# Kernel tuning notes

Hardware: AMD Instinct MI355X
Metric: run time of the kernel (lower is better)

The kernel has to match this reference:

```python
import jax, jax.numpy as jnp
import numpy as np

EPS = 1e-6
H = 12  # num_attention_heads

def _phi(x):
    # feature map used by fast-transformers LinearAttention: elu(x) + 1
    return jax.nn.elu(x) + 1.0

def setup_inputs() -> dict:
    key = jax.random.key(0)
    k1, k2, k3 = jax.random.split(key, 3)
    B, N, D = 32, 1024, 768
    x = jax.random.normal(k1, (B, N, D), dtype=jnp.float32)
    W_qkv = jax.random.normal(k2, (D, 3 * D), dtype=jnp.float32) * (D ** -0.5)
    W_out = jax.random.normal(k3, (D, D), dtype=jnp.float32) * (D ** -0.5)
    b_out = jnp.zeros((D,), dtype=jnp.float32)
    return {"x": x, "W_qkv": W_qkv, "W_out": W_out, "b_out": b_out}

def reference(x, W_qkv, W_out, b_out):
    B, N, D = x.shape
    d = D // H
    # F.pad(x, [0,0,0,1]): append one zero token along sequence
    x_ = jnp.pad(x, ((0, 0), (0, 1), (0, 0)))              # [B, N+1, D]
    qkv = x_ @ W_qkv                                        # [B, N+1, 3D]
    q, k, v = jnp.split(qkv, 3, axis=-1)
    q = q.reshape(B, N + 1, H, d)
    k = k.reshape(B, N + 1, H, d)
    v = v.reshape(B, N + 1, H, d)
    # non-causal linear attention (mask is all-ones -> no masking)
    q = _phi(q)
    k = _phi(k)
    kv = jnp.einsum('bshd,bshm->bhdm', k, v)                # [B, H, d, d]
    z = 1.0 / (jnp.einsum('blhd,bhd->blh', q, k.sum(axis=1)) + EPS)
    out = jnp.einsum('blhd,bhdm,blh->blhm', q, kv, z)       # [B, N+1, H, d]
    out = out.reshape(B, N + 1, D)
    out = out @ W_out + b_out                               # dropout = identity (eval)
    return out[:, :-1, :]                                   # drop padding token
```

## Files before the change

kernel.cpp:

```cpp
#include <hip/hip_runtime.h>
#include <hip/hip_bf16.h>


typedef __bf16 bf16x8 __attribute__((ext_vector_type(8)));
typedef float f32x4 __attribute__((ext_vector_type(4)));

__device__ __forceinline__ ushort f2bf(float f) {
  union { float f; unsigned u; } x; x.f = f;
  unsigned r = x.u + 0x7fffu + ((x.u >> 16) & 1u);
  return (ushort)(r >> 16);
}
__device__ __forceinline__ float bf2f(ushort h) {
  union { unsigned u; float f; } x; x.u = ((unsigned)h) << 16;
  return x.f;
}
__device__ __forceinline__ float bits2f(unsigned u) {
  union { unsigned u; float f; } x; x.u = u;
  return x.f;
}
__device__ __forceinline__ void gload_lds16(const void* g, void* lds) {
  __builtin_amdgcn_global_load_lds((const __attribute__((address_space(1))) void*)g,
                                   (__attribute__((address_space(3))) void*)lds, 16, 0, 0);
}
__device__ __forceinline__ bf16x8 ds_read128(const ushort* p) {
  bf16x8 r;
  asm volatile("ds_read_b128 %0, %1"
               : "=v"(r)
               : "v"((const __attribute__((address_space(3))) ushort*)p));
  return r;
}

__global__ __launch_bounds__(256) void cvt_f32_bf16(const float* __restrict__ in,
                                                    ushort* __restrict__ out, int n4) {
  int i = blockIdx.x * 256 + threadIdx.x;
  if (i >= n4) return;
  float4 v = reinterpret_cast<const float4*>(in)[i];
  ushort4 o;
  o.x = f2bf(v.x); o.y = f2bf(v.y); o.z = f2bf(v.z); o.w = f2bf(v.w);
  reinterpret_cast<ushort4*>(out)[i] = o;
}

__global__ __launch_bounds__(256) void transpose_cvt(const float* __restrict__ src,
                                                     ushort* __restrict__ dst, int R, int C) {
  __shared__ float tile[32][33];
  int bc = blockIdx.x * 32, br = blockIdx.y * 32;
  int tx = threadIdx.x & 31, ty = threadIdx.x >> 5;
  #pragma unroll
  for (int i = 0; i < 32; i += 8)
    tile[ty + i][tx] = src[(size_t)(br + ty + i) * C + (bc + tx)];
  __syncthreads();
  #pragma unroll
  for (int i = 0; i < 32; i += 8)
    dst[(size_t)(bc + ty + i) * R + (br + tx)] = f2bf(tile[tx][ty + i]);
}

template <int MODE>
__global__ __launch_bounds__(512, 2) void gemm256(const ushort* __restrict__ A,
                                                  const ushort* __restrict__ Bt,
                                                  void* __restrict__ C,
                                                  const float* __restrict__ bias,
                                                  int N, int K, int nbx, int cpx) {
  extern __shared__ ushort lds[];
  const int tid = threadIdx.x;
  const int lane = tid & 63;
  const int wid = tid >> 6;
  const int wm = wid >> 2, wn = wid & 3;
  const int laneR = lane & 15, laneS = lane >> 4;

  const int bid = blockIdx.x;
  const int lin = (bid & 7) * cpx + (bid >> 3);
  const int by = lin / nbx, bx = lin - by * nbx;
  const int m0 = by * 256, n0 = bx * 256;
  const int NT = K >> 6;

  const int sr = tid >> 2, ss = tid & 3;
  const int sslot = ss ^ ((sr >> 1) & 3);
  const ushort* Asrc0 = A + (size_t)(m0 + sr) * K + sslot * 8;
  const ushort* Bsrc0 = Bt + (size_t)(n0 + sr) * K + sslot * 8;
  const size_t rowstep = (size_t)128 * K;
  const int ldst0 = tid * 8;

  const int sprime = laneS ^ ((laneR >> 1) & 3);
  const int aoff = (wm * 128 + laneR) * 32 + sprime * 8;
  const int boff = 16384 + (wn * 64 + laneR) * 32 + sprime * 8;

  f32x4 acc[8][4] = {};
  bf16x8 afrX[4], afrY[4], bfrX[4], bfrY[4];

  #define STAGE_HT(SRC, KT, KS, DST)                                              \
    { gload_lds16((SRC) + (KT) * 64 + (KS) * 32,                                  \
                  (DST) + (KS) * 8192 + ldst0);                                   \
      gload_lds16((SRC) + (KT) * 64 + (KS) * 32 + rowstep,                        \
                  (DST) + (KS) * 8192 + 4096 + ldst0); }
  #define SBAR  __builtin_amdgcn_sched_barrier(0)
  #define MFMA16(ACCBASE, AF, BF)                                                 \
    _Pragma("unroll")                                                             \
    for (int ii = 0; ii < 4; ++ii)                                                \
      _Pragma("unroll")                                                           \
      for (int j = 0; j < 4; ++j)                                                 \
        acc[(ACCBASE) + ii][j] =                                                  \
            __builtin_amdgcn_mfma_f32_16x16x32_bf16(AF[ii], BF[j], acc[(ACCBASE) + ii][j], 0, 0, 0);

  {
    ushort* b0 = lds;
    ushort* b1 = lds + 32768;
    STAGE_HT(Asrc0, 0, 0, b0);
    STAGE_HT(Bsrc0, 0, 0, b0 + 16384);
    STAGE_HT(Asrc0, 0, 1, b0);
    STAGE_HT(Bsrc0, 0, 1, b0 + 16384);
    STAGE_HT(Asrc0, 1, 0, b1);
    STAGE_HT(Bsrc0, 1, 0, b1 + 16384);
  }
  asm volatile("s_waitcnt vmcnt(8)" ::: "memory");
  SBAR;
  __builtin_amdgcn_s_barrier();
  SBAR;
  #pragma unroll
  for (int j = 0; j < 4; ++j)
    bfrX[j] = *(const bf16x8*)(lds + boff + j * 512);
  #pragma unroll
  for (int ii = 0; ii < 4; ++ii)
    afrX[ii] = *(const bf16x8*)(lds + aoff + ii * 512);

  for (int t = 0; t < NT; ++t) {
    ushort* cbuf = lds + (t & 1) * 32768;
    ushort* nbuf = lds + ((t & 1) ^ 1) * 32768;
    const int t1 = (t + 1 < NT) ? t + 1 : t;
    const int t2 = (t + 2 < NT) ? t + 2 : t;

    STAGE_HT(Asrc0, t1, 1, nbuf);
    asm volatile("s_waitcnt vmcnt(6)" ::: "memory");
    SBAR;
    #pragma unroll
    for (int ii = 0; ii < 4; ++ii)
      afrY[ii] = *(const bf16x8*)(cbuf + aoff + (4 + ii) * 512);
    SBAR;
    __builtin_amdgcn_s_setprio(1);
    MFMA16(0, afrX, bfrX);
    __builtin_amdgcn_s_setprio(0);
    SBAR;
    __builtin_amdgcn_s_barrier();
    SBAR;

    STAGE_HT(Bsrc0, t1, 1, nbuf + 16384);
    SBAR;
    #pragma unroll
    for (int j = 0; j < 4; ++j)
      bfrY[j] = *(const bf16x8*)(cbuf + 8192 + boff + j * 512);
    #pragma unroll
    for (int ii = 0; ii < 4; ++ii)
      afrX[ii] = *(const bf16x8*)(cbuf + 8192 + aoff + ii * 512);
    SBAR;
    __builtin_amdgcn_s_setprio(1);
    MFMA16(4, afrY, bfrX);
    __builtin_amdgcn_s_setprio(0);
    SBAR;
    __builtin_amdgcn_s_barrier();
    SBAR;

    STAGE_HT(Asrc0, t2, 0, cbuf);
    asm volatile("s_waitcnt vmcnt(6)" ::: "memory");
    SBAR;
    #pragma unroll
    for (int ii = 0; ii < 4; ++ii)
      afrY[ii] = *(const bf16x8*)(cbuf + 8192 + aoff + (4 + ii) * 512);
    SBAR;
    __builtin_amdgcn_s_setprio(1);
    MFMA16(0, afrX, bfrY);
    __builtin_amdgcn_s_setprio(0);
    SBAR;
    __builtin_amdgcn_s_barrier();
    SBAR;

    STAGE_HT(Bsrc0, t2, 0, cbuf + 16384);
    SBAR;
    #pragma unroll
    for (int j = 0; j < 4; ++j)
      bfrX[j] = *(const bf16x8*)(nbuf + boff + j * 512);
    #pragma unroll
    for (int ii = 0; ii < 4; ++ii)
      afrX[ii] = *(const bf16x8*)(nbuf + aoff + ii * 512);
    SBAR;
    __builtin_amdgcn_s_setprio(1);
    MFMA16(4, afrY, bfrY);
    __builtin_amdgcn_s_setprio(0);
    SBAR;
    __builtin_amdgcn_s_barrier();
    SBAR;
  }
  #undef STAGE_HT
  #undef MFMA16
  asm volatile("s_waitcnt vmcnt(0)" ::: "memory");

  #pragma unroll
  for (int i = 0; i < 8; ++i) {
    const int grow0 = m0 + wm * 128 + i * 16 + (laneS << 2);
    #pragma unroll
    for (int j = 0; j < 4; ++j) {
      const int gcol = n0 + wn * 64 + j * 16 + laneR;
      #pragma unroll
      for (int r = 0; r < 4; ++r) {
        float v = acc[i][j][r];
        if (MODE == 0) {
          if (gcol < 1536) v = (v > 0.f) ? (v + 1.f) : __expf(v);
          reinterpret_cast<ushort*>(C)[(size_t)(grow0 + r) * N + gcol] = f2bf(v);
        } else {
          reinterpret_cast<float*>(C)[(size_t)(grow0 + r) * N + gcol] = v + bias[gcol];
        }
      }
    }
  }
}

template <int MODE, int MFR>
__global__ __launch_bounds__(512, 2) void gemm2ph(const ushort* __restrict__ A,
                                                  const ushort* __restrict__ Bt,
                                                  void* __restrict__ C,
                                                  const float* __restrict__ bias,
                                                  int N, int K, int nbx, int cpx) {
  constexpr int BM   = MFR * 32;
  constexpr int ALD  = MFR / 4;
  constexpr int AKS  = BM * 32;
  constexpr int BBASE = BM * 64;
  constexpr int BUFS = (BM + 256) * 64;
  extern __shared__ ushort lds[];
  const int tid = threadIdx.x;
  const int lane = tid & 63;
  const int wid = tid >> 6;
  const int wm = wid >> 2, wn = wid & 3;
  const int laneR = lane & 15, laneS = lane >> 4;

  const int bid = blockIdx.x;
  const int lin = (bid & 7) * cpx + (bid >> 3);
  const int by = lin / nbx, bx = lin - by * nbx;
  const int m0 = by * BM, n0 = bx * 256;
  const int NT = K >> 6;

  const int sr = tid >> 2, ss = tid & 3;
  const int sslot = ss ^ ((sr >> 1) & 3);
  const ushort* Asrc0 = A + (size_t)(m0 + sr) * K + sslot * 8;
  const ushort* Bsrc0 = Bt + (size_t)(n0 + sr) * K + sslot * 8;
  const size_t rowstep = (size_t)128 * K;
  const int ldst0 = tid * 8;

  const int sprime = laneS ^ ((laneR >> 1) & 3);
  const int aoff = (wm * (MFR * 16) + laneR) * 32 + sprime * 8;
  const int boff = BBASE + (wn * 64 + laneR) * 32 + sprime * 8;

  f32x4 acc[MFR][4] = {};
  bf16x8 afr[MFR], bfr[4];

  #define STAGE_K(KT, KS, DB)                                                     \
    { _Pragma("unroll")                                                           \
      for (int L = 0; L < ALD; ++L)                                               \
        gload_lds16(Asrc0 + (KT) * 64 + (KS) * 32 + (size_t)L * rowstep,          \
                    lds + (DB) + (KS) * AKS + L * 4096 + ldst0);                  \
      _Pragma("unroll")                                                           \
      for (int L = 0; L < 2; ++L)                                                 \
        gload_lds16(Bsrc0 + (KT) * 64 + (KS) * 32 + (size_t)L * rowstep,          \
                    lds + (DB) + BBASE + (KS) * 8192 + L * 4096 + ldst0); }
  #define SBAR  __builtin_amdgcn_sched_barrier(0)
  #define VMCNT_WAIT                                                              \
    if constexpr (MFR == 8) asm volatile("s_waitcnt vmcnt(8)" ::: "memory");      \
    else                    asm volatile("s_waitcnt vmcnt(6)" ::: "memory");
  #define PHASE_SYNC                                                              \
    SBAR;                                                                         \
    __builtin_amdgcn_s_barrier();                                                 \
    asm volatile("s_waitcnt lgkmcnt(0)");                                         \
    SBAR;
  #define PHASE_END                                                               \
    SBAR;                                                                         \
    __builtin_amdgcn_s_barrier();                                                 \
    SBAR;
  #define MFMA_CL                                                                 \
    __builtin_amdgcn_s_setprio(1);                                                \
    _Pragma("unroll")                                                             \
    for (int ii = 0; ii < MFR; ++ii)                                              \
      _Pragma("unroll")                                                           \
      for (int j = 0; j < 4; ++j)                                                 \
        acc[ii][j] =                                                              \
            __builtin_amdgcn_mfma_f32_16x16x32_bf16(afr[ii], bfr[j], acc[ii][j], 0, 0, 0); \
    __builtin_amdgcn_s_setprio(0);

  STAGE_K(0, 0, 0);
  STAGE_K(0, 1, 0);
  STAGE_K(1, 0, BUFS);
  VMCNT_WAIT;
  SBAR;
  __builtin_amdgcn_s_barrier();
  SBAR;

  for (int t = 0; t < NT; ++t) {
    const int cb = (t & 1) * BUFS;
    const int nb = BUFS - cb;
    const int t1 = (t + 1 < NT) ? t + 1 : t;
    const int t2 = (t + 2 < NT) ? t + 2 : t;

    #pragma unroll
    for (int j = 0; j < 4; ++j) bfr[j] = ds_read128(lds + cb + boff + j * 512);
    #pragma unroll
    for (int ii = 0; ii < MFR; ++ii) afr[ii] = ds_read128(lds + cb + aoff + ii * 512);
    STAGE_K(t1, 1, nb);
    VMCNT_WAIT;
    PHASE_SYNC;
    MFMA_CL;
    PHASE_END;

    #pragma unroll
    for (int j = 0; j < 4; ++j) bfr[j] = ds_read128(lds + cb + 8192 + boff + j * 512);
    #pragma unroll
    for (int ii = 0; ii < MFR; ++ii) afr[ii] = ds_read128(lds + cb + AKS + aoff + ii * 512);
    STAGE_K(t2, 0, cb);
    VMCNT_WAIT;
    PHASE_SYNC;
    MFMA_CL;
    PHASE_END;
  }
  #undef STAGE_K
  #undef MFMA_CL
  #undef PHASE_SYNC
  #undef PHASE_END
  #undef VMCNT_WAIT
  asm volatile("s_waitcnt vmcnt(0)" ::: "memory");

  #pragma unroll
  for (int i = 0; i < MFR; ++i) {
    const int grow0 = m0 + wm * (MFR * 16) + i * 16 + (laneS << 2);
    #pragma unroll
    for (int j = 0; j < 4; ++j) {
      const int gcol = n0 + wn * 64 + j * 16 + laneR;
      #pragma unroll
      for (int r = 0; r < 4; ++r) {
        float v = acc[i][j][r];
        if (MODE == 0) {
          if (gcol < 1536) v = (v > 0.f) ? (v + 1.f) : __expf(v);
          reinterpret_cast<ushort*>(C)[(size_t)(grow0 + r) * N + gcol] = f2bf(v);
        } else {
          reinterpret_cast<float*>(C)[(size_t)(grow0 + r) * N + gcol] = v + bias[gcol];
        }
      }
    }
  }
}

__global__ __launch_bounds__(256) void kv_partial(const ushort* __restrict__ qkv,
                                                  float* __restrict__ kv_part,
                                                  float* __restrict__ ks_part) {
  const int blk = blockIdx.x;
  const int bh = blk >> 2, sp = blk & 3;
  const int b = bh / 12, h = bh % 12;
  const int tid = threadIdx.x;
  __shared__ float Ks[32 * 68];
  __shared__ float Vs[32 * 68];
  float acc[4][4] = {};
  float kacc[4] = {};
  const int dq0 = (tid & 15) * 4, mq0 = (tid >> 4) * 4;
  const int r = tid >> 3, o = (tid & 7) * 8;
  for (int st = 0; st < 256; st += 32) {
    const size_t rowbase = (size_t)(b * 1024 + sp * 256 + st + r) * 2304 + h * 64 + o;
    int4 kraw = *reinterpret_cast<const int4*>(qkv + rowbase + 768);
    int4 vraw = *reinterpret_cast<const int4*>(qkv + rowbase + 1536);
    float kf[8], vf[8];
    {
      const unsigned* kw = reinterpret_cast<const unsigned*>(&kraw);
      const unsigned* vw = reinterpret_cast<const unsigned*>(&vraw);
      #pragma unroll
      for (int w = 0; w < 4; ++w) {
        kf[2 * w]     = bits2f(kw[w] << 16);
        kf[2 * w + 1] = bits2f(kw[w] & 0xffff0000u);
        vf[2 * w]     = bits2f(vw[w] << 16);
        vf[2 * w + 1] = bits2f(vw[w] & 0xffff0000u);
      }
    }
    __syncthreads();
    #pragma unroll
    for (int w = 0; w < 8; ++w) {
      Ks[r * 68 + o + w] = kf[w];
      Vs[r * 68 + o + w] = vf[w];
    }
    __syncthreads();
    #pragma unroll 8
    for (int s = 0; s < 32; ++s) {
      f32x4 kk = *reinterpret_cast<const f32x4*>(&Ks[s * 68 + dq0]);
      f32x4 vv = *reinterpret_cast<const f32x4*>(&Vs[s * 68 + mq0]);
      #pragma unroll
      for (int jm = 0; jm < 4; ++jm)
        #pragma unroll
        for (int id = 0; id < 4; ++id)
          acc[jm][id] += vv[jm] * kk[id];
      if (mq0 == 0) {
        #pragma unroll
        for (int id = 0; id < 4; ++id) kacc[id] += kk[id];
      }
    }
  }
  float* kvp = kv_part + ((size_t)sp * 384 + bh) * 4096;
  #pragma unroll
  for (int jm = 0; jm < 4; ++jm)
    #pragma unroll
    for (int id = 0; id < 4; ++id)
      kvp[(mq0 + jm) * 64 + dq0 + id] = acc[jm][id];
  if (mq0 == 0) {
    #pragma unroll
    for (int id = 0; id < 4; ++id)
      ks_part[((size_t)sp * 384 + bh) * 64 + dq0 + id] = kacc[id];
  }
}

__global__ __launch_bounds__(256) void kv_reduce(const float* __restrict__ kv_part,
                                                 const float* __restrict__ ks_part,
                                                 ushort* __restrict__ kv_bf,
                                                 float* __restrict__ ksum) {
  int i = blockIdx.x * 256 + threadIdx.x;
  if (i < 384 * 4096) {
    float s = 0.f;
    #pragma unroll
    for (int p = 0; p < 4; ++p) s += kv_part[(size_t)p * (384 * 4096) + i];
    kv_bf[i] = f2bf(s);
  }
  if (i < 384 * 64) {
    float s = 1.0f;
    #pragma unroll
    for (int p = 0; p < 4; ++p) s += ks_part[(size_t)p * (384 * 64) + i];
    ksum[i] = s;
  }
}

__global__ __launch_bounds__(256) void attn_kernel(const ushort* __restrict__ qkv,
                                                   const ushort* __restrict__ kv_bf,
                                                   const float* __restrict__ ksum,
                                                   ushort* __restrict__ attn) {
  const int blk = blockIdx.x;
  const int bh = blk >> 3, tb = blk & 7;
  const int b = bh / 12, h = bh % 12;
  const int row0 = b * 1024 + tb * 128;
  __shared__ ushort Qs[128 * 64];
  __shared__ ushort KVs[64 * 64];
  __shared__ float zs[128];
  __shared__ float ks_lds[64];
  const int tid = threadIdx.x;
  const int lane = tid & 63, w = tid >> 6;
  #pragma unroll
  for (int j = 0; j < 4; ++j) {
    int c = j * 256 + tid;
    gload_lds16(qkv + (size_t)(row0 + (c >> 3)) * 2304 + h * 64 + (c & 7) * 8, &Qs[c * 8]);
  }
  #pragma unroll
  for (int j = 0; j < 2; ++j) {
    int c = j * 256 + tid;
    gload_lds16(kv_bf + (size_t)bh * 4096 + c * 8, &KVs[c * 8]);
  }
  if (tid < 64) ks_lds[tid] = ksum[bh * 64 + tid];
  asm volatile("s_waitcnt vmcnt(0)" ::: "memory");
  __syncthreads();
  if (tid < 128) {
    float d = 0.f;
    #pragma unroll 8
    for (int e = 0; e < 64; ++e) d += bf2f(Qs[tid * 64 + e]) * ks_lds[e];
    zs[tid] = 1.f / (d + 1e-6f);
  }
  __syncthreads();
  f32x4 acc[2][4] = {};
  #pragma unroll
  for (int ks = 0; ks < 2; ++ks) {
    bf16x8 a[2], bb[4];
    #pragma unroll
    for (int i = 0; i < 2; ++i)
      a[i] = *reinterpret_cast<const bf16x8*>(&Qs[(w * 32 + i * 16 + (lane & 15)) * 64 + ks * 32 + (lane >> 4) * 8]);
    #pragma unroll
    for (int j = 0; j < 4; ++j)
      bb[j] = *reinterpret_cast<const bf16x8*>(&KVs[(j * 16 + (lane & 15)) * 64 + ks * 32 + (lane >> 4) * 8]);
    #pragma unroll
    for (int i = 0; i < 2; ++i)
      #pragma unroll
      for (int j = 0; j < 4; ++j)
        acc[i][j] = __builtin_amdgcn_mfma_f32_16x16x32_bf16(a[i], bb[j], acc[i][j], 0, 0, 0);
  }
  #pragma unroll
  for (int i = 0; i < 2; ++i) {
    const int t0 = w * 32 + i * 16 + ((lane >> 4) << 2);
    #pragma unroll
    for (int j = 0; j < 4; ++j) {
      const int m = j * 16 + (lane & 15);
      #pragma unroll
      for (int r = 0; r < 4; ++r) {
        float v = acc[i][j][r] * zs[t0 + r];
        attn[(size_t)(row0 + t0 + r) * 768 + h * 64 + m] = f2bf(v);
      }
    }
  }
}

extern "C" void kernel_launch(void* const* d_in, const int* in_sizes, int n_in,
                              void* d_out, int out_size, void* d_ws, size_t ws_size,
                              hipStream_t stream) {
  (void)in_sizes; (void)n_in; (void)out_size; (void)ws_size;
  const float* x    = (const float*)d_in[0];
  const float* Wqkv = (const float*)d_in[1];
  const float* Wout = (const float*)d_in[2];
  const float* bout = (const float*)d_in[3];
  float* out = (float*)d_out;
  char* ws = (char*)d_ws;

  ushort* xbf    = (ushort*)(ws);
  ushort* wqkvT  = (ushort*)(ws + 50331648);
  ushort* woutT  = (ushort*)(ws + 53870592);
  ushort* qkv    = (ushort*)(ws + 55050240);
  float*  ksp    = (float*) (ws + 206045184);
  ushort* kvbf   = (ushort*)(ws + 206438400);
  float*  ksum   = (float*) (ws + 209584128);
  float*  kvpart = (float*)(ws);
  ushort* attn   = (ushort*)(ws);

  static const int LDS1 = 131072;
  static const int LDS2 = 98304;
  hipFuncSetAttribute(reinterpret_cast<const void*>(&gemm256<0>),
                      hipFuncAttributeMaxDynamicSharedMemorySize, LDS1);
  hipFuncSetAttribute(reinterpret_cast<const void*>(&gemm2ph<1, 4>),
                      hipFuncAttributeMaxDynamicSharedMemorySize, LDS2);

  cvt_f32_bf16<<<24576, 256, 0, stream>>>(x, xbf, 6291456);
  transpose_cvt<<<dim3(72, 24), 256, 0, stream>>>(Wqkv, wqkvT, 768, 2304);
  transpose_cvt<<<dim3(24, 24), 256, 0, stream>>>(Wout, woutT, 768, 768);
  gemm256<0><<<1152, 512, LDS1, stream>>>(xbf, wqkvT, qkv, nullptr, 2304, 768, 9, 144);
  kv_partial<<<1536, 256, 0, stream>>>(qkv, kvpart, ksp);
  kv_reduce<<<6144, 256, 0, stream>>>(kvpart, ksp, kvbf, ksum);
  attn_kernel<<<3072, 256, 0, stream>>>(qkv, kvbf, ksum, attn);
  gemm2ph<1, 4><<<768, 512, LDS2, stream>>>(attn, woutT, out, bout, 768, 768, 3, 96);
}
```

Before: 304.1 us.

## Replace 256x256 QKV GEMM with 64x256 tiles loading B directly into registers

The QKV projection GEMM moves from 256x256 tiles with 8 waves and both operands staged in LDS to 64x256 tiles with 4 waves. In the new kernel only A goes through LDS, and each wave loads its B fragments straight from global memory into registers. The aim is more blocks, higher occupancy and less LDS pressure and barrier cost. In exchange, global and L2 traffic for B rises because it is reused across fewer rows, and arithmetic intensity per block drops.

```diff
diff --git a/kernel.cpp b/kernel.cpp
--- a/kernel.cpp
+++ b/kernel.cpp
@@ -27,6 +27,13 @@
   asm volatile("ds_read_b128 %0, %1"
                : "=v"(r)
                : "v"((const __attribute__((address_space(3))) ushort*)p));
+  return r;
+}
+__device__ __forceinline__ bf16x8 gload128(const ushort* p) {
+  bf16x8 r;
+  asm volatile("global_load_dwordx4 %0, %1, off"
+               : "=v"(r)
+               : "v"(p));
   return r;
 }
 
@@ -55,146 +62,105 @@
 }
 
 template <int MODE>
-__global__ __launch_bounds__(512, 2) void gemm256(const ushort* __restrict__ A,
-                                                  const ushort* __restrict__ Bt,
-                                                  void* __restrict__ C,
-                                                  const float* __restrict__ bias,
-                                                  int N, int K, int nbx, int cpx) {
-  extern __shared__ ushort lds[];
+__global__ __launch_bounds__(256, 3) void gemm64(const ushort* __restrict__ A,
+                                                 const ushort* __restrict__ Bt,
+                                                 void* __restrict__ C,
+                                                 const float* __restrict__ bias,
+                                                 int N, int K, int nbx, int cpx) {
+  __shared__ ushort As[2][4096];
   const int tid = threadIdx.x;
   const int lane = tid & 63;
-  const int wid = tid >> 6;
-  const int wm = wid >> 2, wn = wid & 3;
+  const int wn = tid >> 6;
   const int laneR = lane & 15, laneS = lane >> 4;
 
   const int bid = blockIdx.x;
   const int lin = (bid & 7) * cpx + (bid >> 3);
   const int by = lin / nbx, bx = lin - by * nbx;
-  const int m0 = by * 256, n0 = bx * 256;
+  const int m0 = by * 64, n0 = bx * 256;
   const int NT = K >> 6;
 
   const int sr = tid >> 2, ss = tid & 3;
   const int sslot = ss ^ ((sr >> 1) & 3);
-  const ushort* Asrc0 = A + (size_t)(m0 + sr) * K + sslot * 8;
-  const ushort* Bsrc0 = Bt + (size_t)(n0 + sr) * K + sslot * 8;
-  const size_t rowstep = (size_t)128 * K;
-  const int ldst0 = tid * 8;
+  const ushort* Asrc = A + (size_t)(m0 + sr) * K + sslot * 8;
+  const int ldst = tid * 8;
 
   const int sprime = laneS ^ ((laneR >> 1) & 3);
-  const int aoff = (wm * 128 + laneR) * 32 + sprime * 8;
-  const int boff = 16384 + (wn * 64 + laneR) * 32 + sprime * 8;
-
-  f32x4 acc[8][4] = {};
-  bf16x8 afrX[4], afrY[4], bfrX[4], bfrY[4];
-
-  #define STAGE_HT(SRC, KT, KS, DST)                                              \
-    { gload_lds16((SRC) + (KT) * 64 + (KS) * 32,                                  \
-                  (DST) + (KS) * 8192 + ldst0);                                   \
-      gload_lds16((SRC) + (KT) * 64 + (KS) * 32 + rowstep,                        \
-                  (DST) + (KS) * 8192 + 4096 + ldst0); }
+  const int aoff = laneR * 32 + sprime * 8;
+
+  const ushort* Bb0 = Bt + (size_t)(n0 + wn * 64 + laneR) * K + laneS * 8;
+  const size_t jstep = (size_t)16 * K;
+
+  f32x4 acc[4][4] = {};
+  bf16x8 afr[4], bfrX[4], bfrY[4];
+
   #define SBAR  __builtin_amdgcn_sched_barrier(0)
-  #define MFMA16(ACCBASE, AF, BF)                                                 \
+  #define MFMA16(AF, BF)                                                          \
+    __builtin_amdgcn_s_setprio(1);                                                \
     _Pragma("unroll")                                                             \
     for (int ii = 0; ii < 4; ++ii)                                                \
       _Pragma("unroll")                                                           \
       for (int j = 0; j < 4; ++j)                                                 \
-        acc[(ACCBASE) + ii][j] =                                                  \
-            __builtin_amdgcn_mfma_f32_16x16x32_bf16(AF[ii], BF[j], acc[(ACCBASE) + ii][j], 0, 0, 0);
-
-  {
-    ushort* b0 = lds;
-    ushort* b1 = lds + 32768;
-    STAGE_HT(Asrc0, 0, 0, b0);
-    STAGE_HT(Bsrc0, 0, 0, b0 + 16384);
-    STAGE_HT(Asrc0, 0, 1, b0);
-    STAGE_HT(Bsrc0, 0, 1, b0 + 16384);
-    STAGE_HT(Asrc0, 1, 0, b1);
-    STAGE_HT(Bsrc0, 1, 0, b1 + 16384);
-  }
-  asm volatile("s_waitcnt vmcnt(8)" ::: "memory");
+        acc[ii][j] =                                                              \
+            __builtin_amdgcn_mfma_f32_16x16x32_bf16(AF[ii], BF[j], acc[ii][j], 0, 0, 0); \
+    __builtin_amdgcn_s_setprio(0);
+
+  gload_lds16(Asrc,      &As[0][0]    + ldst);
+  gload_lds16(Asrc + 32, &As[0][2048] + ldst);
+  gload_lds16(Asrc + 64, &As[1][0]    + ldst);
+  #pragma unroll
+  for (int j = 0; j < 4; ++j)
+    bfrX[j] = gload128(Bb0 + (size_t)j * jstep);
+  asm volatile("s_waitcnt vmcnt(0)" ::: "memory");
   SBAR;
   __builtin_amdgcn_s_barrier();
   SBAR;
-  #pragma unroll
-  for (int j = 0; j < 4; ++j)
-    bfrX[j] = *(const bf16x8*)(lds + boff + j * 512);
-  #pragma unroll
-  for (int ii = 0; ii < 4; ++ii)
-    afrX[ii] = *(const bf16x8*)(lds + aoff + ii * 512);
 
   for (int t = 0; t < NT; ++t) {
-    ushort* cbuf = lds + (t & 1) * 32768;
-    ushort* nbuf = lds + ((t & 1) ^ 1) * 32768;
+    ushort* cb = &As[t & 1][0];
+    ushort* nb = &As[(t & 1) ^ 1][0];
     const int t1 = (t + 1 < NT) ? t + 1 : t;
     const int t2 = (t + 2 < NT) ? t + 2 : t;
 
-    STAGE_HT(Asrc0, t1, 1, nbuf);
+    #pragma unroll
+    for (int i = 0; i < 4; ++i)
+      afr[i] = ds_read128(cb + aoff + i * 512);
+    #pragma unroll
+    for (int j = 0; j < 4; ++j)
+      bfrY[j] = gload128(Bb0 + (size_t)j * jstep + t * 64 + 32);
+    gload_lds16(Asrc + t1 * 64 + 32, nb + 2048 + ldst);
     asm volatile("s_waitcnt vmcnt(6)" ::: "memory");
     SBAR;
-    #pragma unroll
-    for (int ii = 0; ii < 4; ++ii)
-      afrY[ii] = *(const bf16x8*)(cbuf + aoff + (4 + ii) * 512);
-    SBAR;
-    __builtin_amdgcn_s_setprio(1);
-    MFMA16(0, afrX, bfrX);
-    __builtin_amdgcn_s_setprio(0);
-    SBAR;
     __builtin_amdgcn_s_barrier();
-    SBAR;
-
-    STAGE_HT(Bsrc0, t1, 1, nbuf + 16384);
-    SBAR;
+    asm volatile("s_waitcnt lgkmcnt(0)");
+    SBAR;
+    MFMA16(afr, bfrX);
+    SBAR;
+    __builtin_amdgcn_s_barrier();
+    SBAR;
+
+    #pragma unroll
+    for (int i = 0; i < 4; ++i)
+      afr[i] = ds_read128(cb + 2048 + aoff + i * 512);
     #pragma unroll
     for (int j = 0; j < 4; ++j)
-      bfrY[j] = *(const bf16x8*)(cbuf + 8192 + boff + j * 512);
-    #pragma unroll
-    for (int ii = 0; ii < 4; ++ii)
-      afrX[ii] = *(const bf16x8*)(cbuf + 8192 + aoff + ii * 512);
-    SBAR;
-    __builtin_amdgcn_s_setprio(1);
-    MFMA16(4, afrY, bfrX);
-    __builtin_amdgcn_s_setprio(0);
+      bfrX[j] = gload128(Bb0 + (size_t)j * jstep + t1 * 64);
+    gload_lds16(Asrc + t2 * 64, cb + ldst);
+    asm volatile("s_waitcnt vmcnt(6)" ::: "memory");
     SBAR;
     __builtin_amdgcn_s_barrier();
-    SBAR;
-
-    STAGE_HT(Asrc0, t2, 0, cbuf);
-    asm volatile("s_waitcnt vmcnt(6)" ::: "memory");
-    SBAR;
-    #pragma unroll
-    for (int ii = 0; ii < 4; ++ii)
-      afrY[ii] = *(const bf16x8*)(cbuf + 8192 + aoff + (4 + ii) * 512);
-    SBAR;
-    __builtin_amdgcn_s_setprio(1);
-    MFMA16(0, afrX, bfrY);
-    __builtin_amdgcn_s_setprio(0);
+    asm volatile("s_waitcnt lgkmcnt(0)");
+    SBAR;
+    MFMA16(afr, bfrY);
     SBAR;
     __builtin_amdgcn_s_barrier();
     SBAR;
-
-    STAGE_HT(Bsrc0, t2, 0, cbuf + 16384);
-    SBAR;
-    #pragma unroll
-    for (int j = 0; j < 4; ++j)
-      bfrX[j] = *(const bf16x8*)(nbuf + boff + j * 512);
-    #pragma unroll
-    for (int ii = 0; ii < 4; ++ii)
-      afrX[ii] = *(const bf16x8*)(nbuf + aoff + ii * 512);
-    SBAR;
-    __builtin_amdgcn_s_setprio(1);
-    MFMA16(4, afrY, bfrY);
-    __builtin_amdgcn_s_setprio(0);
-    SBAR;
-    __builtin_amdgcn_s_barrier();
-    SBAR;
-  }
-  #undef STAGE_HT
+  }
   #undef MFMA16
   asm volatile("s_waitcnt vmcnt(0)" ::: "memory");
 
   #pragma unroll
-  for (int i = 0; i < 8; ++i) {
-    const int grow0 = m0 + wm * 128 + i * 16 + (laneS << 2);
+  for (int i = 0; i < 4; ++i) {
+    const int grow0 = m0 + i * 16 + (laneS << 2);
     #pragma unroll
     for (int j = 0; j < 4; ++j) {
       const int gcol = n0 + wn * 64 + j * 16 + laneR;
@@ -259,7 +225,6 @@
       for (int L = 0; L < 2; ++L)                                                 \
         gload_lds16(Bsrc0 + (KT) * 64 + (KS) * 32 + (size_t)L * rowstep,          \
                     lds + (DB) + BBASE + (KS) * 8192 + L * 4096 + ldst0); }
-  #define SBAR  __builtin_amdgcn_sched_barrier(0)
   #define VMCNT_WAIT                                                              \
     if constexpr (MFR == 8) asm volatile("s_waitcnt vmcnt(8)" ::: "memory");      \
     else                    asm volatile("s_waitcnt vmcnt(6)" ::: "memory");
@@ -512,17 +477,14 @@
   float*  kvpart = (float*)(ws);
   ushort* attn   = (ushort*)(ws);
 
-  static const int LDS1 = 131072;
   static const int LDS2 = 98304;
-  hipFuncSetAttribute(reinterpret_cast<const void*>(&gemm256<0>),
-                      hipFuncAttributeMaxDynamicSharedMemorySize, LDS1);
   hipFuncSetAttribute(reinterpret_cast<const void*>(&gemm2ph<1, 4>),
                       hipFuncAttributeMaxDynamicSharedMemorySize, LDS2);
 
   cvt_f32_bf16<<<24576, 256, 0, stream>>>(x, xbf, 6291456);
   transpose_cvt<<<dim3(72, 24), 256, 0, stream>>>(Wqkv, wqkvT, 768, 2304);
   transpose_cvt<<<dim3(24, 24), 256, 0, stream>>>(Wout, woutT, 768, 768);
-  gemm256<0><<<1152, 512, LDS1, stream>>>(xbf, wqkvT, qkv, nullptr, 2304, 768, 9, 144);
+  gemm64<0><<<4608, 256, 0, stream>>>(xbf, wqkvT, qkv, nullptr, 2304, 768, 9, 576);
   kv_partial<<<1536, 256, 0, stream>>>(qkv, kvpart, ksp);
   kv_reduce<<<6144, 256, 0, stream>>>(kvpart, ksp, kvbf, ksum);
   attn_kernel<<<3072, 256, 0, stream>>>(qkv, kvbf, ksum, attn);
```

Result: slower. 398.2 us (+30.9%).

## Stage GEMM tiles through registers with explicit ds_write instead of direct-to-LDS loads

Applied to the files above, without the earlier changes.

Replaces the global_load_lds direct-to-LDS staging in the 256x256 QKV GEMM with global_load_dwordx4 into registers followed by ds_write_b128. The loads are issued one phase ahead and written to LDS in a later phase, with an extra barrier per phase before the MFMA block. The aim is finer control over load/compute overlap, at the cost of more VGPRs, extra LDS write instructions and additional barriers. The register-held tiles could also lower occupancy.

```diff
diff --git a/kernel.cpp b/kernel.cpp
--- a/kernel.cpp
+++ b/kernel.cpp
@@ -27,6 +27,18 @@
   asm volatile("ds_read_b128 %0, %1"
                : "=v"(r)
                : "v"((const __attribute__((address_space(3))) ushort*)p));
+  return r;
+}
+__device__ __forceinline__ void ds_write128(ushort* p, bf16x8 v) {
+  asm volatile("ds_write_b128 %0, %1"
+               :: "v"((__attribute__((address_space(3))) ushort*)p), "v"(v)
+               : "memory");
+}
+__device__ __forceinline__ bf16x8 gload128(const ushort* p) {
+  bf16x8 r;
+  asm volatile("global_load_dwordx4 %0, %1, off"
+               : "=v"(r)
+               : "v"(p));
   return r;
 }
 
@@ -86,12 +98,8 @@
 
   f32x4 acc[8][4] = {};
   bf16x8 afrX[4], afrY[4], bfrX[4], bfrY[4];
-
-  #define STAGE_HT(SRC, KT, KS, DST)                                              \
-    { gload_lds16((SRC) + (KT) * 64 + (KS) * 32,                                  \
-                  (DST) + (KS) * 8192 + ldst0);                                   \
-      gload_lds16((SRC) + (KT) * 64 + (KS) * 32 + rowstep,                        \
-                  (DST) + (KS) * 8192 + 4096 + ldst0); }
+  bf16x8 r0a, r0b, r1a, r1b, r2a, r2b, r3a, r3b;
+
   #define SBAR  __builtin_amdgcn_sched_barrier(0)
   #define MFMA16(ACCBASE, AF, BF)                                                 \
     _Pragma("unroll")                                                             \
@@ -101,17 +109,22 @@
         acc[(ACCBASE) + ii][j] =                                                  \
             __builtin_amdgcn_mfma_f32_16x16x32_bf16(AF[ii], BF[j], acc[(ACCBASE) + ii][j], 0, 0, 0);
 
-  {
-    ushort* b0 = lds;
-    ushort* b1 = lds + 32768;
-    STAGE_HT(Asrc0, 0, 0, b0);
-    STAGE_HT(Bsrc0, 0, 0, b0 + 16384);
-    STAGE_HT(Asrc0, 0, 1, b0);
-    STAGE_HT(Bsrc0, 0, 1, b0 + 16384);
-    STAGE_HT(Asrc0, 1, 0, b1);
-    STAGE_HT(Bsrc0, 1, 0, b1 + 16384);
-  }
-  asm volatile("s_waitcnt vmcnt(8)" ::: "memory");
+  r0a = gload128(Asrc0);            r0b = gload128(Asrc0 + rowstep);
+  r1a = gload128(Bsrc0);            r1b = gload128(Bsrc0 + rowstep);
+  asm volatile("s_waitcnt vmcnt(0)" ::: "memory");
+  ds_write128(lds + ldst0, r0a);            ds_write128(lds + 4096 + ldst0, r0b);
+  ds_write128(lds + 16384 + ldst0, r1a);    ds_write128(lds + 16384 + 4096 + ldst0, r1b);
+  r0a = gload128(Asrc0 + 32);       r0b = gload128(Asrc0 + 32 + rowstep);
+  r1a = gload128(Bsrc0 + 32);       r1b = gload128(Bsrc0 + 32 + rowstep);
+  asm volatile("s_waitcnt vmcnt(0)" ::: "memory");
+  ds_write128(lds + 8192 + ldst0, r0a);     ds_write128(lds + 8192 + 4096 + ldst0, r0b);
+  ds_write128(lds + 16384 + 8192 + ldst0, r1a);
+  ds_write128(lds + 16384 + 8192 + 4096 + ldst0, r1b);
+  r2a = gload128(Asrc0 + 64);       r2b = gload128(Asrc0 + 64 + rowstep);
+  asm volatile("s_waitcnt vmcnt(0)" ::: "memory");
+  ds_write128(lds + 32768 + ldst0, r2a);    ds_write128(lds + 32768 + 4096 + ldst0, r2b);
+  r3a = gload128(Bsrc0 + 64);       r3b = gload128(Bsrc0 + 64 + rowstep);
+  asm volatile("s_waitcnt lgkmcnt(0)" ::: "memory");
   SBAR;
   __builtin_amdgcn_s_barrier();
   SBAR;
@@ -128,12 +141,17 @@
     const int t1 = (t + 1 < NT) ? t + 1 : t;
     const int t2 = (t + 2 < NT) ? t + 2 : t;
 
-    STAGE_HT(Asrc0, t1, 1, nbuf);
-    asm volatile("s_waitcnt vmcnt(6)" ::: "memory");
-    SBAR;
     #pragma unroll
     for (int ii = 0; ii < 4; ++ii)
       afrY[ii] = *(const bf16x8*)(cbuf + aoff + (4 + ii) * 512);
+    r0a = gload128(Asrc0 + t1 * 64 + 32);
+    r0b = gload128(Asrc0 + t1 * 64 + 32 + rowstep);
+    asm volatile("s_waitcnt vmcnt(2)" ::: "memory");
+    ds_write128(nbuf + 16384 + ldst0, r3a);
+    ds_write128(nbuf + 16384 + 4096 + ldst0, r3b);
+    asm volatile("s_waitcnt lgkmcnt(0)" ::: "memory");
+    SBAR;
+    __builtin_amdgcn_s_barrier();
     SBAR;
     __builtin_amdgcn_s_setprio(1);
     MFMA16(0, afrX, bfrX);
@@ -142,14 +160,20 @@
     __builtin_amdgcn_s_barrier();
     SBAR;
 
-    STAGE_HT(Bsrc0, t1, 1, nbuf + 16384);
-    SBAR;
     #pragma unroll
     for (int j = 0; j < 4; ++j)
       bfrY[j] = *(const bf16x8*)(cbuf + 8192 + boff + j * 512);
     #pragma unroll
     for (int ii = 0; ii < 4; ++ii)
       afrX[ii] = *(const bf16x8*)(cbuf + 8192 + aoff + ii * 512);
+    r1a = gload128(Bsrc0 + t1 * 64 + 32);
+    r1b = gload128(Bsrc0 + t1 * 64 + 32 + rowstep);
+    asm volatile("s_waitcnt vmcnt(2)" ::: "memory");
+    ds_write128(nbuf + 8192 + ldst0, r0a);
+    ds_write128(nbuf + 8192 + 4096 + ldst0, r0b);
+    asm volatile("s_waitcnt lgkmcnt(0)" ::: "memory");
+    SBAR;
+    __builtin_amdgcn_s_barrier();
     SBAR;
     __builtin_amdgcn_s_setprio(1);
     MFMA16(4, afrY, bfrX);
@@ -158,12 +182,17 @@
     __builtin_amdgcn_s_barrier();
     SBAR;
 
-    STAGE_HT(Asrc0, t2, 0, cbuf);
-    asm volatile("s_waitcnt vmcnt(6)" ::: "memory");
-    SBAR;
     #pragma unroll
     for (int ii = 0; ii < 4; ++ii)
       afrY[ii] = *(const bf16x8*)(cbuf + 8192 + aoff + (4 + ii) * 512);
+    r2a = gload128(Asrc0 + t2 * 64);
+    r2b = gload128(Asrc0 + t2 * 64 + rowstep);
+    asm volatile("s_waitcnt vmcnt(2)" ::: "memory");
+    ds_write128(nbuf + 16384 + 8192 + ldst0, r1a);
+    ds_write128(nbuf + 16384 + 8192 + 4096 + ldst0, r1b);
+    asm volatile("s_waitcnt lgkmcnt(0)" ::: "memory");
+    SBAR;
+    __builtin_amdgcn_s_barrier();
     SBAR;
     __builtin_amdgcn_s_setprio(1);
     MFMA16(0, afrX, bfrY);
@@ -172,14 +201,20 @@
     __builtin_amdgcn_s_barrier();
     SBAR;
 
-    STAGE_HT(Bsrc0, t2, 0, cbuf + 16384);
-    SBAR;
     #pragma unroll
     for (int j = 0; j < 4; ++j)
       bfrX[j] = *(const bf16x8*)(nbuf + boff + j * 512);
     #pragma unroll
     for (int ii = 0; ii < 4; ++ii)
       afrX[ii] = *(const bf16x8*)(nbuf + aoff + ii * 512);
+    r3a = gload128(Bsrc0 + t2 * 64);
+    r3b = gload128(Bsrc0 + t2 * 64 + rowstep);
+    asm volatile("s_waitcnt vmcnt(2)" ::: "memory");
+    ds_write128(cbuf + ldst0, r2a);
+    ds_write128(cbuf + 4096 + ldst0, r2b);
+    asm volatile("s_waitcnt lgkmcnt(0)" ::: "memory");
+    SBAR;
+    __builtin_amdgcn_s_barrier();
     SBAR;
     __builtin_amdgcn_s_setprio(1);
     MFMA16(4, afrY, bfrY);
@@ -188,7 +223,6 @@
     __builtin_amdgcn_s_barrier();
     SBAR;
   }
-  #undef STAGE_HT
   #undef MFMA16
   asm volatile("s_waitcnt vmcnt(0)" ::: "memory");
 
@@ -259,7 +293,6 @@
       for (int L = 0; L < 2; ++L)                                                 \
         gload_lds16(Bsrc0 + (KT) * 64 + (KS) * 32 + (size_t)L * rowstep,          \
                     lds + (DB) + BBASE + (KS) * 8192 + L * 4096 + ldst0); }
-  #define SBAR  __builtin_amdgcn_sched_barrier(0)
   #define VMCNT_WAIT                                                              \
     if constexpr (MFR == 8) asm volatile("s_waitcnt vmcnt(8)" ::: "memory");      \
     else                    asm volatile("s_waitcnt vmcnt(6)" ::: "memory");
```

Result: slower. 318.1 us (+4.6%).
